# Performance work log

Measured on AMD Instinct MI355X. Metric: run time of the kernel, lower is better.

The kernel has to match this reference:

```python
import jax, jax.numpy as jnp
import numpy as np

N, E, H, L, R, NG = 8192, 131072, 256, 3, 128, 64
NUM_ELEMENTS = 80
CUTOFF = 12.0
INV_SQRT_2 = 1.0 / np.sqrt(2.0)
INV_SQRT_3 = 1.0 / np.sqrt(3.0)
INV_SQRT_H = 1.0 / np.sqrt(H)


def _glorot(key, shape):
    fan_in, fan_out = shape[-2], shape[-1]
    return jax.random.normal(key, shape, jnp.float32) * np.sqrt(2.0 / (fan_in + fan_out))


def setup_inputs():
    key = jax.random.key(0)
    ks = jax.random.split(key, 24)
    pos = jax.random.normal(ks[0], (N, 3), jnp.float32) * 5.0
    z = jax.random.randint(ks[1], (N,), 0, NUM_ELEMENTS)
    src = jax.random.randint(ks[2], (E,), 0, N)
    off = jax.random.randint(ks[3], (E,), 1, N)
    dst = (src + off) % N  # guarantee no self-loops (dist > 0)
    edge_index = jnp.stack([src, dst])
    batch = jnp.sort(jax.random.randint(ks[4], (N,), 0, NG))
    return {
        "pos": pos,
        "atom_emb": jax.random.normal(ks[5], (NUM_ELEMENTS, H), jnp.float32),
        "ln_w": jnp.ones((L, H), jnp.float32),
        "ln_b": jnp.zeros((L, H), jnp.float32),
        "xp_w1": _glorot(ks[6], (L, H, H)),
        "xp_b1": jnp.zeros((L, H), jnp.float32),
        "xp_w2": _glorot(ks[7], (L, H, 3 * H)),
        "xp_b2": jnp.zeros((L, 3 * H), jnp.float32),
        "rbf_w": _glorot(ks[8], (L, R, 3 * H)),
        "rbf_b": jnp.zeros((L, 3 * H), jnp.float32),
        "vec_w": _glorot(ks[9], (L, H, 2 * H)),
        "xv_w1": _glorot(ks[10], (L, 2 * H, H)),
        "xv_b1": jnp.zeros((L, H), jnp.float32),
        "xv_w2": _glorot(ks[11], (L, H, 3 * H)),
        "xv_b2": jnp.zeros((L, 3 * H), jnp.float32),
        "oe_w1": _glorot(ks[12], (H, H // 2)),
        "oe_b1": jnp.zeros((H // 2,), jnp.float32),
        "oe_w2": _glorot(ks[13], (H // 2, 1)),
        "oe_b2": jnp.zeros((1,), jnp.float32),
        "z": z,
        "edge_index": edge_index,
        "batch": batch,
    }


def _gaussian_rbf(dist):
    offset = jnp.linspace(0.0, CUTOFF, R)
    coeff = -0.5 / (offset[1] - offset[0]) ** 2
    return jnp.exp(coeff * (dist[:, None] - offset[None, :]) ** 2)  # [E, R]


def _layernorm(x, w, b):
    mu = x.mean(-1, keepdims=True)
    var = x.var(-1, keepdims=True)
    return (x - mu) / jnp.sqrt(var + 1e-5) * w + b


def reference(pos, atom_emb, ln_w, ln_b, xp_w1, xp_b1, xp_w2, xp_b2,
              rbf_w, rbf_b, vec_w, xv_w1, xv_b1, xv_w2, xv_b2,
              oe_w1, oe_b1, oe_w2, oe_b2, z, edge_index, batch):
    src, dst = edge_index[0], edge_index[1]
    rel = pos[src] - pos[dst]                       # [E, 3]
    dist = jnp.sqrt((rel ** 2).sum(-1))             # [E]
    edge_rbf = _gaussian_rbf(dist)                  # [E, R]
    edge_vector = rel / dist[:, None]               # [E, 3] unit vectors

    x = atom_emb[z]                                 # [N, H]
    vec = jnp.zeros((N, 3, H), x.dtype)

    for l in range(L):
        # ---- PaiNNMessage ----
        xh = _layernorm(x, ln_w[l], ln_b[l])
        xh = jax.nn.silu(xh @ xp_w1[l] + xp_b1[l]) @ xp_w2[l] + xp_b2[l]  # [N, 3H]
        rbfh = edge_rbf @ rbf_w[l] + rbf_b[l]                             # [E, 3H]
        m = xh[src] * rbfh
        mx, xh2, xh3 = jnp.split(m, 3, axis=-1)
        xh2 = xh2 * INV_SQRT_3
        mvec = (vec[src] * xh2[:, None, :] + xh3[:, None, :] * edge_vector[:, :, None]) * INV_SQRT_H
        dx = jax.ops.segment_sum(mx, dst, num_segments=N)
        dvec = jax.ops.segment_sum(mvec, dst, num_segments=N)
        x = (x + dx) * INV_SQRT_2
        vec = vec + dvec

        # ---- PaiNNUpdate ----
        vp = vec @ vec_w[l]                          # [N, 3, 2H]
        vec1, vec2 = jnp.split(vp, 2, axis=-1)
        vec_dot = (vec1 * vec2).sum(axis=1) * INV_SQRT_H           # [N, H]
        vnorm = jnp.sqrt((vec2 ** 2).sum(axis=1) + 1e-8)           # [N, H]
        h = jnp.concatenate([x, vnorm], axis=-1)
        h = jax.nn.silu(h @ xv_w1[l] + xv_b1[l]) @ xv_w2[l] + xv_b2[l]
        xv1, xv2, xv3 = jnp.split(h, 3, axis=-1)
        dx = (xv1 + xv2 * vec_dot) * INV_SQRT_2
        dvec = xv3[:, None, :] * vec1
        x = (x + dx) * INV_SQRT_2
        vec = vec + dvec

    # ---- energy head: per-atom MLP then per-molecule sum ----
    per_atom = jax.nn.silu(x @ oe_w1 + oe_b1) @ oe_w2 + oe_b2      # [N, 1]
    energy = jax.ops.segment_sum(per_atom, batch, num_segments=NG)  # [NG, 1]
    return energy
```

## Files before the change

kernel.cpp:

```cpp
#include <hip/hip_runtime.h>
#include <hip/hip_bf16.h>
#include <math.h>

#define NN 8192
#define EE 131072
#define HH 256
#define LL 3
#define RR 128
#define NGG 64
#define MSG_WAVES 16

typedef __attribute__((ext_vector_type(8))) short bf16x8;
typedef __attribute__((ext_vector_type(4))) float f32x4;
typedef unsigned short u16;

#if defined(__has_builtin)
#if __has_builtin(__builtin_amdgcn_fdot2_f32_bf16)
#define HAVE_FDOT2 1
typedef __attribute__((ext_vector_type(2))) __bf16 bf16x2_t;
union BU { unsigned u; bf16x2_t v; };
#endif
#if __has_builtin(__builtin_amdgcn_global_load_lds)
#define HAVE_GLL 1
#endif
#endif

union U4 { ushort4 v; unsigned short a[4]; };
union U8 { uint4 v; unsigned short a[8]; unsigned w[4]; };

__device__ __forceinline__ float silu(float v) { return v / (1.0f + expf(-v)); }
__device__ __forceinline__ float b2f(unsigned short u) { return __uint_as_float(((unsigned)u) << 16); }
__device__ __forceinline__ unsigned short f2b(float f) {
    unsigned u = __float_as_uint(f);
    u += 0x7fff + ((u >> 16) & 1);
    return (unsigned short)(u >> 16);
}

constexpr float kInvSqrt2 = 0.70710678118654752440f;
constexpr float kInvSqrt3 = 0.57735026918962576451f;
constexpr float kInvSqrtH = 0.0625f;

__global__ void k_zero(float* __restrict__ p, int n4) {
    int i = blockIdx.x * 256 + threadIdx.x;
    if (i < n4) ((float4*)p)[i] = make_float4(0.f, 0.f, 0.f, 0.f);
}

__global__ __launch_bounds__(256) void k_wt_all(
    const float* __restrict__ xp_w1, const float* __restrict__ xp_w2,
    const float* __restrict__ rbf_w, const float* __restrict__ vec_w,
    const float* __restrict__ xv_w1, const float* __restrict__ xv_w2,
    const float* __restrict__ oe_w1,
    u16* __restrict__ xp_w1T, u16* __restrict__ xp_w2T, u16* __restrict__ rbf_wP,
    u16* __restrict__ vec_wT, u16* __restrict__ xv_w1T, u16* __restrict__ xv_w2T,
    u16* __restrict__ oe_w1T) {
    int bid = blockIdx.x;
    const float* src; u16* dst; int K, N, t, pairmode = 0;
    if (bid < 2400) {
        int l = bid / 800, r = bid % 800;
        if (r < 64)       { src = xp_w1 + (size_t)l * 65536;  dst = xp_w1T + (size_t)l * 65536;  K = 256; N = 256; t = r; }
        else if (r < 256) { src = xp_w2 + (size_t)l * 196608; dst = xp_w2T + (size_t)l * 196608; K = 256; N = 768; t = r - 64; }
        else if (r < 352) { src = rbf_w + (size_t)l * 98304;  dst = rbf_wP + (size_t)l * 98304;  K = 128; N = 768; t = r - 256; pairmode = 1; }
        else if (r < 480) { src = vec_w + (size_t)l * 131072; dst = vec_wT + (size_t)l * 131072; K = 256; N = 512; t = r - 352; }
        else if (r < 608) { src = xv_w1 + (size_t)l * 131072; dst = xv_w1T + (size_t)l * 131072; K = 512; N = 256; t = r - 480; }
        else              { src = xv_w2 + (size_t)l * 196608; dst = xv_w2T + (size_t)l * 196608; K = 256; N = 768; t = r - 608; }
    } else {
        src = oe_w1; dst = oe_w1T; K = 256; N = 128; t = bid - 2400;
    }
    int nx = N >> 5;
    int bn = (t % nx) * 32, bk = (t / nx) * 32;
    int tx = threadIdx.x & 31, ty = threadIdx.x >> 5;
    if (pairmode) {
#pragma unroll
        for (int i = 0; i < 32; i += 8) {
            int k = bk + ty + i, n = bn + tx;
            dst[(size_t)(k >> 1) * 1536 + n * 2 + (k & 1)] = f2b(src[(size_t)k * N + n]);
        }
        return;
    }
    __shared__ float tile[32][33];
#pragma unroll
    for (int i = 0; i < 32; i += 8)
        tile[ty + i][tx] = src[(size_t)(bk + ty + i) * N + bn + tx];
    __syncthreads();
#pragma unroll
    for (int i = 0; i < 32; i += 8)
        dst[(size_t)(bn + ty + i) * K + bk + tx] = f2b(tile[tx][ty + i]);
}

__global__ void k_init_ln(const float* __restrict__ emb, const int* __restrict__ z,
                          const float* __restrict__ w, const float* __restrict__ b,
                          float* __restrict__ x, u16* __restrict__ xlnb) {
    int n = blockIdx.x, t = threadIdx.x;
    float v = emb[z[n] * HH + t];
    x[(size_t)n * HH + t] = v;
    float s = v, q = v * v;
#pragma unroll
    for (int m = 32; m >= 1; m >>= 1) {
        s += __shfl_xor(s, m, 64);
        q += __shfl_xor(q, m, 64);
    }
    __shared__ float s_sum[4], s_sq[4];
    int wid = t >> 6;
    if ((t & 63) == 0) { s_sum[wid] = s; s_sq[wid] = q; }
    __syncthreads();
    float S = s_sum[0] + s_sum[1] + s_sum[2] + s_sum[3];
    float Q = s_sq[0] + s_sq[1] + s_sq[2] + s_sq[3];
    float mu = S * (1.0f / HH);
    float var = Q * (1.0f / HH) - mu * mu;
    float rs = rsqrtf(var + 1e-5f);
    xlnb[(size_t)n * HH + t] = f2b((v - mu) * rs * w[t] + b[t]);
}

__global__ void k_geom_hist(const float* __restrict__ pos, const int* __restrict__ ei,
                            float* __restrict__ ev, int* __restrict__ deg) {
    int e = blockIdx.x * 256 + threadIdx.x;
    if (e >= EE) return;
    int s = ei[e], d = ei[EE + e];
    float rx = pos[s * 3 + 0] - pos[d * 3 + 0];
    float ry = pos[s * 3 + 1] - pos[d * 3 + 1];
    float rz = pos[s * 3 + 2] - pos[d * 3 + 2];
    float dist = sqrtf(rx * rx + ry * ry + rz * rz);
    float inv = 1.0f / dist;
    ((float4*)ev)[e] = make_float4(rx * inv, ry * inv, rz * inv, dist);
    atomicAdd(&deg[d], 1);
}

__global__ void k_scan1(const int* __restrict__ deg, int* __restrict__ row_ptr,
                        int* __restrict__ csum) {
    __shared__ int buf[256];
    int t = threadIdx.x, base = blockIdx.x * 256;
    int v = deg[base + t];
    buf[t] = v;
    __syncthreads();
    for (int ofs = 1; ofs < 256; ofs <<= 1) {
        int add = (t >= ofs) ? buf[t - ofs] : 0;
        __syncthreads();
        buf[t] += add;
        __syncthreads();
    }
    row_ptr[base + t] = buf[t] - v;
    if (t == 255) csum[blockIdx.x] = buf[t];
}
__global__ void k_scan2(int* __restrict__ csum) {
    if (threadIdx.x == 0) {
        int acc = 0;
        for (int i = 0; i < 32; ++i) { int v = csum[i]; csum[i] = acc; acc += v; }
        csum[32] = acc;
    }
}
__global__ void k_scan3(const int* __restrict__ csum, int* __restrict__ row_ptr,
                        int* __restrict__ fill) {
    int i = blockIdx.x * 256 + threadIdx.x;
    int v = row_ptr[i] + csum[i >> 8];
    row_ptr[i] = v;
    fill[i] = v;
    if (i == 0) row_ptr[NN] = csum[32];
}

__global__ void k_sort(const int* __restrict__ deg, int* __restrict__ dorder) {
    __shared__ int bins[256];
    __shared__ int base[256];
    int t = threadIdx.x;
    bins[t] = 0;
    __syncthreads();
    for (int d = t; d < NN; d += 256) {
        int b = deg[d]; b = b > 255 ? 255 : b;
        atomicAdd(&bins[b], 1);
    }
    __syncthreads();
    if (t == 0) {
        int acc = 0;
        for (int k = 255; k >= 0; --k) { base[k] = acc; acc += bins[k]; }
    }
    __syncthreads();
    bins[t] = 0;
    __syncthreads();
    for (int d = t; d < NN; d += 256) {
        int b = deg[d]; b = b > 255 ? 255 : b;
        int p = atomicAdd(&bins[b], 1);
        dorder[base[b] + p] = d;
    }
}

__global__ void k_scatter(const int* __restrict__ ei, const float* __restrict__ ev,
                          int* __restrict__ fill, int* __restrict__ srcp,
                          float4* __restrict__ evp, int* __restrict__ kptab,
                          unsigned* __restrict__ gtab) {
    int e = blockIdx.x * 256 + threadIdx.x;
    if (e >= EE) return;
    int d = ei[EE + e];
    int pos = atomicAdd(&fill[d], 1);
    float4 e4 = ((const float4*)ev)[e];
    srcp[pos] = ei[e];
    evp[pos] = e4;
    const float step = 12.0f / 127.0f;
    const float coeff = -0.5f / (step * step);
    float dist = e4.w;
    int k0 = ((int)floorf(dist / step) - 3) & ~1;
    k0 = k0 < 0 ? 0 : (k0 > 120 ? 120 : k0);
    float g[8];
#pragma unroll
    for (int k = 0; k < 8; ++k) {
        float t = dist - (k0 + k) * step;
        g[k] = expf(coeff * t * t);
    }
    kptab[pos] = k0 >> 1;
    unsigned g0 = (unsigned)f2b(g[0]) | ((unsigned)f2b(g[1]) << 16);
    unsigned g1 = (unsigned)f2b(g[2]) | ((unsigned)f2b(g[3]) << 16);
    unsigned g2 = (unsigned)f2b(g[4]) | ((unsigned)f2b(g[5]) << 16);
    unsigned g3 = (unsigned)f2b(g[6]) | ((unsigned)f2b(g[7]) << 16);
    ((uint4*)gtab)[pos] = make_uint4(g0, g1, g2, g3);
}

template <int OUT_BF16, int ACT, int TN>
__global__ __launch_bounds__(256) void k_gemm(
    const u16* __restrict__ A, const u16* __restrict__ BT,
    const float* __restrict__ bias, void* __restrict__ C, int M, int K, int N) {
    __shared__ u16 As[64 * 64];
    __shared__ u16 Bs[TN * 64];
    const int NJ = TN / 32;
    int tid = threadIdx.x;
    int wave = tid >> 6, lane = tid & 63;
    int bm = blockIdx.y * 64, bn = blockIdx.x * TN;
    int wm = (wave & 1) * 32, wn = (wave >> 1) * (TN / 2);
    int lm = lane & 15;
    int kg = lane >> 4;
    f32x4 acc[2][NJ] = {};

    for (int k0 = 0; k0 < K; k0 += 64) {
#pragma unroll
        for (int it = 0; it < 2; ++it) {
            int idx = it * 256 + tid;
            int r = idx >> 3, seg = idx & 7;
#ifdef HAVE_GLL
            __builtin_amdgcn_global_load_lds(
                (const unsigned*)&A[(size_t)(bm + r) * K + k0 + seg * 8],
                (unsigned*)&As[idx * 8], 16, 0, 0);
#else
            *(uint4*)&As[idx * 8] = *(const uint4*)&A[(size_t)(bm + r) * K + k0 + seg * 8];
#endif
        }
#pragma unroll
        for (int it = 0; it < TN / 32; ++it) {
            int idx = it * 256 + tid;
            int r = idx >> 3, seg = idx & 7;
#ifdef HAVE_GLL
            __builtin_amdgcn_global_load_lds(
                (const unsigned*)&BT[(size_t)(bn + r) * K + k0 + seg * 8],
                (unsigned*)&Bs[idx * 8], 16, 0, 0);
#else
            *(uint4*)&Bs[idx * 8] = *(const uint4*)&BT[(size_t)(bn + r) * K + k0 + seg * 8];
#endif
        }
        __syncthreads();
#pragma unroll
        for (int kh = 0; kh < 2; ++kh) {
            bf16x8 af[2], bfr[NJ];
#pragma unroll
            for (int i = 0; i < 2; ++i)
                af[i] = *(const bf16x8*)&As[(wm + i * 16 + lm) * 64 + kh * 32 + kg * 8];
#pragma unroll
            for (int j = 0; j < NJ; ++j)
                bfr[j] = *(const bf16x8*)&Bs[(wn + j * 16 + lm) * 64 + kh * 32 + kg * 8];
#pragma unroll
            for (int i = 0; i < 2; ++i)
#pragma unroll
                for (int j = 0; j < NJ; ++j)
                    acc[i][j] = __builtin_amdgcn_mfma_f32_16x16x32_bf16(af[i], bfr[j], acc[i][j], 0, 0, 0);
        }
        __syncthreads();
    }

#pragma unroll
    for (int j = 0; j < NJ; ++j) {
        int col = bn + wn + j * 16 + lm;
        float bv = bias ? bias[col] : 0.f;
#pragma unroll
        for (int i = 0; i < 2; ++i) {
            int row0 = bm + wm + i * 16 + kg * 4;
#pragma unroll
            for (int r = 0; r < 4; ++r) {
                float v = acc[i][j][r] + bv;
                if (ACT) v = silu(v);
                if (OUT_BF16)
                    ((u16*)C)[(size_t)(row0 + r) * N + col] = f2b(v);
                else
                    ((float*)C)[(size_t)(row0 + r) * N + col] = v;
            }
        }
    }
}

__global__ __launch_bounds__(1024) void k_msg(
    const u16* __restrict__ xhb, const u16* __restrict__ vinb,
    const int* __restrict__ srcp, const float4* __restrict__ evp,
    const int* __restrict__ row_ptr, const int* __restrict__ kptab,
    const unsigned* __restrict__ gtab, const u16* __restrict__ WP ,
    const float* __restrict__ rbias, float* __restrict__ x,
    const float* __restrict__ vin, u16* __restrict__ vecMb,
    const int* __restrict__ dorder) {
    __shared__ u16 Wp[64 * 512];
    int tid = threadIdx.x;
    int wave = tid >> 6, lane = tid & 63;
    int c0 = lane * 4;
    int d = dorder[blockIdx.x * MSG_WAVES + wave];
    int E0 = row_ptr[d], E1 = row_ptr[d + 1];
    float accv[3][4] = {};

#pragma unroll
    for (int p = 0; p < 3; ++p) {
        __syncthreads();
#pragma unroll
        for (int it = 0; it < 4; ++it) {
            int idx = it * 1024 + tid;
            int r = idx >> 6;
            int c8 = (idx & 63) * 8;
            *(uint4*)&Wp[r * 512 + c8] =
                *(const uint4*)&WP[(size_t)r * 1536 + p * 512 + c8];
        }
        __syncthreads();
        float4 bb = ((const float4*)(rbias + p * 256))[lane];
        float bias4[4] = {bb.x, bb.y, bb.z, bb.w};
        float accx[4] = {};

        int kp_n = 0; uint4 gt_n = make_uint4(0, 0, 0, 0);
        U4 X_n; U4 V0_n, V1_n, V2_n; float4 ev_n;
        X_n.v = make_ushort4(0, 0, 0, 0);
        V0_n = X_n; V1_n = X_n; V2_n = X_n;
        ev_n = make_float4(0.f, 0.f, 0.f, 0.f);
        if (E0 < E1) {
            int s0 = srcp[E0];
            kp_n = kptab[E0];
            gt_n = ((const uint4*)gtab)[E0];
            X_n.v = *(const ushort4*)(xhb + (size_t)s0 * 768 + p * 256 + c0);
            if (p == 1) {
                V0_n.v = *(const ushort4*)(vinb + (size_t)s0 * 768 + c0);
                V1_n.v = *(const ushort4*)(vinb + (size_t)s0 * 768 + 256 + c0);
                V2_n.v = *(const ushort4*)(vinb + (size_t)s0 * 768 + 512 + c0);
            }
            if (p == 2) ev_n = evp[E0];
        }
        for (int j = E0; j < E1; ++j) {
            int kp = kp_n;
            uint4 gt = gt_n;
            U4 X = X_n, V0 = V0_n, V1 = V1_n, V2 = V2_n;
            float4 ev4 = ev_n;
            if (j + 1 < E1) {
                int s2 = srcp[j + 1];
                kp_n = kptab[j + 1];
                gt_n = ((const uint4*)gtab)[j + 1];
                X_n.v = *(const ushort4*)(xhb + (size_t)s2 * 768 + p * 256 + c0);
                if (p == 1) {
                    V0_n.v = *(const ushort4*)(vinb + (size_t)s2 * 768 + c0);
                    V1_n.v = *(const ushort4*)(vinb + (size_t)s2 * 768 + 256 + c0);
                    V2_n.v = *(const ushort4*)(vinb + (size_t)s2 * 768 + 512 + c0);
                }
                if (p == 2) ev_n = evp[j + 1];
            }
            unsigned gp0 = gt.x, gp1 = gt.y, gp2 = gt.z, gp3 = gt.w;
            float rr[4] = {bias4[0], bias4[1], bias4[2], bias4[3]};
            {
                U8 w0, w1, w2, w3;
                w0.v = *(const uint4*)&Wp[(kp + 0) * 512 + c0 * 2];
                w1.v = *(const uint4*)&Wp[(kp + 1) * 512 + c0 * 2];
                w2.v = *(const uint4*)&Wp[(kp + 2) * 512 + c0 * 2];
                w3.v = *(const uint4*)&Wp[(kp + 3) * 512 + c0 * 2];
#ifdef HAVE_FDOT2
                BU g0; g0.u = gp0; BU g1; g1.u = gp1;
                BU g2; g2.u = gp2; BU g3; g3.u = gp3;
#pragma unroll
                for (int c = 0; c < 4; ++c) {
                    BU a; a.u = w0.w[c];
                    rr[c] = __builtin_amdgcn_fdot2_f32_bf16(a.v, g0.v, rr[c], false);
                    a.u = w1.w[c];
                    rr[c] = __builtin_amdgcn_fdot2_f32_bf16(a.v, g1.v, rr[c], false);
                    a.u = w2.w[c];
                    rr[c] = __builtin_amdgcn_fdot2_f32_bf16(a.v, g2.v, rr[c], false);
                    a.u = w3.w[c];
                    rr[c] = __builtin_amdgcn_fdot2_f32_bf16(a.v, g3.v, rr[c], false);
                }
#else
                float ge0 = b2f((u16)(gp0 & 0xffff)), go0 = b2f((u16)(gp0 >> 16));
                float ge1 = b2f((u16)(gp1 & 0xffff)), go1 = b2f((u16)(gp1 >> 16));
                float ge2 = b2f((u16)(gp2 & 0xffff)), go2 = b2f((u16)(gp2 >> 16));
                float ge3 = b2f((u16)(gp3 & 0xffff)), go3 = b2f((u16)(gp3 >> 16));
#pragma unroll
                for (int c = 0; c < 4; ++c) {
                    rr[c] += ge0 * b2f(w0.a[2 * c]) + go0 * b2f(w0.a[2 * c + 1]);
                    rr[c] += ge1 * b2f(w1.a[2 * c]) + go1 * b2f(w1.a[2 * c + 1]);
                    rr[c] += ge2 * b2f(w2.a[2 * c]) + go2 * b2f(w2.a[2 * c + 1]);
                    rr[c] += ge3 * b2f(w3.a[2 * c]) + go3 * b2f(w3.a[2 * c + 1]);
                }
#endif
            }
            if (p == 0) {
#pragma unroll
                for (int c = 0; c < 4; ++c) accx[c] += b2f(X.a[c]) * rr[c];
            } else if (p == 1) {
#pragma unroll
                for (int c = 0; c < 4; ++c) {
                    float m1 = b2f(X.a[c]) * rr[c] * kInvSqrt3;
                    accv[0][c] += b2f(V0.a[c]) * m1;
                    accv[1][c] += b2f(V1.a[c]) * m1;
                    accv[2][c] += b2f(V2.a[c]) * m1;
                }
            } else {
#pragma unroll
                for (int c = 0; c < 4; ++c) {
                    float m2 = b2f(X.a[c]) * rr[c];
                    accv[0][c] += m2 * ev4.x;
                    accv[1][c] += m2 * ev4.y;
                    accv[2][c] += m2 * ev4.z;
                }
            }
        }
        if (p == 0) {
            size_t xi = (size_t)d * 256 + c0;
            float4 xv = *(const float4*)&x[xi];
            xv.x = (xv.x + accx[0]) * kInvSqrt2;
            xv.y = (xv.y + accx[1]) * kInvSqrt2;
            xv.z = (xv.z + accx[2]) * kInvSqrt2;
            xv.w = (xv.w + accx[3]) * kInvSqrt2;
            *(float4*)&x[xi] = xv;
        }
    }
#pragma unroll
    for (int k = 0; k < 3; ++k) {
        size_t idx = (size_t)d * 768 + k * 256 + c0;
        float4 vv = *(const float4*)&vin[idx];
        ushort4 u;
        u.x = f2b(vv.x + accv[k][0] * kInvSqrtH);
        u.y = f2b(vv.y + accv[k][1] * kInvSqrtH);
        u.z = f2b(vv.z + accv[k][2] * kInvSqrtH);
        u.w = f2b(vv.w + accv[k][3] * kInvSqrtH);
        *(ushort4*)&vecMb[idx] = u;
    }
}

__global__ void k_vecdot(const u16* __restrict__ vp, const float* __restrict__ x,
                         float* __restrict__ vec_dot, u16* __restrict__ hcat) {
    int idx = blockIdx.x * 256 + threadIdx.x;
    int n = idx >> 5, lg = idx & 31;
    int c0 = lg * 8;
    const u16* p = vp + (size_t)n * 1536;
    float ds[8] = {}, qs[8] = {};
#pragma unroll
    for (int k = 0; k < 3; ++k) {
        uint4 a = *(const uint4*)&p[k * 512 + c0];
        uint4 b = *(const uint4*)&p[k * 512 + 256 + c0];
        const unsigned* aw = (const unsigned*)&a;
        const unsigned* bw = (const unsigned*)&b;
#pragma unroll
        for (int w = 0; w < 4; ++w) {
            float a0 = __uint_as_float(aw[w] << 16);
            float a1 = __uint_as_float(aw[w] & 0xffff0000u);
            float b0 = __uint_as_float(bw[w] << 16);
            float b1 = __uint_as_float(bw[w] & 0xffff0000u);
            ds[2 * w]     += a0 * b0;  qs[2 * w]     += b0 * b0;
            ds[2 * w + 1] += a1 * b1;  qs[2 * w + 1] += b1 * b1;
        }
    }
    size_t vo = (size_t)n * 256 + c0;
    *(float4*)&vec_dot[vo] =
        make_float4(ds[0] * kInvSqrtH, ds[1] * kInvSqrtH, ds[2] * kInvSqrtH, ds[3] * kInvSqrtH);
    *(float4*)&vec_dot[vo + 4] =
        make_float4(ds[4] * kInvSqrtH, ds[5] * kInvSqrtH, ds[6] * kInvSqrtH, ds[7] * kInvSqrtH);
    float4 x0 = *(const float4*)&x[vo];
    float4 x1 = *(const float4*)&x[vo + 4];
    *(ushort4*)&hcat[(size_t)n * 512 + c0] =
        make_ushort4(f2b(x0.x), f2b(x0.y), f2b(x0.z), f2b(x0.w));
    *(ushort4*)&hcat[(size_t)n * 512 + c0 + 4] =
        make_ushort4(f2b(x1.x), f2b(x1.y), f2b(x1.z), f2b(x1.w));
    *(ushort4*)&hcat[(size_t)n * 512 + 256 + c0] =
        make_ushort4(f2b(sqrtf(qs[0] + 1e-8f)), f2b(sqrtf(qs[1] + 1e-8f)),
                     f2b(sqrtf(qs[2] + 1e-8f)), f2b(sqrtf(qs[3] + 1e-8f)));
    *(ushort4*)&hcat[(size_t)n * 512 + 256 + c0 + 4] =
        make_ushort4(f2b(sqrtf(qs[4] + 1e-8f)), f2b(sqrtf(qs[5] + 1e-8f)),
                     f2b(sqrtf(qs[6] + 1e-8f)), f2b(sqrtf(qs[7] + 1e-8f)));
}

__global__ void k_update_out(const u16* __restrict__ hout, const float* __restrict__ vec_dot,
                             const u16* __restrict__ vp, float* __restrict__ x,
                             const u16* __restrict__ vecMb, float* __restrict__ vfin,
                             u16* __restrict__ vb,
                             const float* __restrict__ lnw, const float* __restrict__ lnb,
                             u16* __restrict__ xout) {
    int idx = blockIdx.x * 256 + threadIdx.x;
    int n = idx >> 5, lg = idx & 31;
    int c0 = lg * 8;
    size_t hb = (size_t)n * 768;
    uint4 H1 = *(const uint4*)&hout[hb + c0];
    uint4 H2 = *(const uint4*)&hout[hb + 256 + c0];
    uint4 H3 = *(const uint4*)&hout[hb + 512 + c0];
    const unsigned* h1w = (const unsigned*)&H1;
    const unsigned* h2w = (const unsigned*)&H2;
    const unsigned* h3w = (const unsigned*)&H3;
    size_t xo = (size_t)n * 256 + c0;
    float4 vd0 = *(const float4*)&vec_dot[xo];
    float4 vd1 = *(const float4*)&vec_dot[xo + 4];
    float vd[8] = {vd0.x, vd0.y, vd0.z, vd0.w, vd1.x, vd1.y, vd1.z, vd1.w};
    float4 x0 = *(const float4*)&x[xo];
    float4 x1 = *(const float4*)&x[xo + 4];
    float xv[8] = {x0.x, x0.y, x0.z, x0.w, x1.x, x1.y, x1.z, x1.w};
    float nx[8], xv3[8];
#pragma unroll
    for (int w = 0; w < 4; ++w) {
        float a1 = __uint_as_float(h1w[w] << 16), b1 = __uint_as_float(h1w[w] & 0xffff0000u);
        float a2 = __uint_as_float(h2w[w] << 16), b2v = __uint_as_float(h2w[w] & 0xffff0000u);
        nx[2 * w]     = (xv[2 * w]     + (a1 + a2  * vd[2 * w])     * kInvSqrt2) * kInvSqrt2;
        nx[2 * w + 1] = (xv[2 * w + 1] + (b1 + b2v * vd[2 * w + 1]) * kInvSqrt2) * kInvSqrt2;
        xv3[2 * w]     = __uint_as_float(h3w[w] << 16);
        xv3[2 * w + 1] = __uint_as_float(h3w[w] & 0xffff0000u);
    }
    *(float4*)&x[xo]     = make_float4(nx[0], nx[1], nx[2], nx[3]);
    *(float4*)&x[xo + 4] = make_float4(nx[4], nx[5], nx[6], nx[7]);
#pragma unroll
    for (int k = 0; k < 3; ++k) {
        size_t vo = hb + k * 256 + c0;
        uint4 VM = *(const uint4*)&vecMb[vo];
        uint4 VP = *(const uint4*)&vp[(size_t)n * 1536 + k * 512 + c0];
        const unsigned* vmw = (const unsigned*)&VM;
        const unsigned* vpw = (const unsigned*)&VP;
        float nv[8];
#pragma unroll
        for (int w = 0; w < 4; ++w) {
            nv[2 * w]     = __uint_as_float(vmw[w] << 16)
                          + xv3[2 * w]     * __uint_as_float(vpw[w] << 16);
            nv[2 * w + 1] = __uint_as_float(vmw[w] & 0xffff0000u)
                          + xv3[2 * w + 1] * __uint_as_float(vpw[w] & 0xffff0000u);
        }
        *(float4*)&vfin[vo]     = make_float4(nv[0], nv[1], nv[2], nv[3]);
        *(float4*)&vfin[vo + 4] = make_float4(nv[4], nv[5], nv[6], nv[7]);
        *(ushort4*)&vb[vo]     = make_ushort4(f2b(nv[0]), f2b(nv[1]), f2b(nv[2]), f2b(nv[3]));
        *(ushort4*)&vb[vo + 4] = make_ushort4(f2b(nv[4]), f2b(nv[5]), f2b(nv[6]), f2b(nv[7]));
    }
    if (lnw) {
        float s = 0.f, q = 0.f;
#pragma unroll
        for (int c = 0; c < 8; ++c) { s += nx[c]; q += nx[c] * nx[c]; }
#pragma unroll
        for (int m = 16; m >= 1; m >>= 1) {
            s += __shfl_xor(s, m, 64);
            q += __shfl_xor(q, m, 64);
        }
        float mu = s * (1.0f / HH);
        float var = q * (1.0f / HH) - mu * mu;
        float rs = rsqrtf(var + 1e-5f);
        float4 w0 = *(const float4*)&lnw[c0], w1 = *(const float4*)&lnw[c0 + 4];
        float4 bb0 = *(const float4*)&lnb[c0], bb1 = *(const float4*)&lnb[c0 + 4];
        float lw[8] = {w0.x, w0.y, w0.z, w0.w, w1.x, w1.y, w1.z, w1.w};
        float lb[8] = {bb0.x, bb0.y, bb0.z, bb0.w, bb1.x, bb1.y, bb1.z, bb1.w};
        u16 o[8];
#pragma unroll
        for (int c = 0; c < 8; ++c) o[c] = f2b((nx[c] - mu) * rs * lw[c] + lb[c]);
        *(ushort4*)&xout[xo]     = make_ushort4(o[0], o[1], o[2], o[3]);
        *(ushort4*)&xout[xo + 4] = make_ushort4(o[4], o[5], o[6], o[7]);
    } else {
        *(ushort4*)&xout[xo]     = make_ushort4(f2b(nx[0]), f2b(nx[1]), f2b(nx[2]), f2b(nx[3]));
        *(ushort4*)&xout[xo + 4] = make_ushort4(f2b(nx[4]), f2b(nx[5]), f2b(nx[6]), f2b(nx[7]));
    }
}

__global__ void k_energy2(const float* __restrict__ h, const float* __restrict__ w2,
                          const float* __restrict__ b2, const int* __restrict__ batch,
                          float* __restrict__ out) {
    __shared__ float g[NGG];
    int t = threadIdx.x;
    if (t < NGG) g[t] = 0.f;
    __syncthreads();
    int a = blockIdx.x * 256 + t;
    const float4* hr = (const float4*)(h + (size_t)a * 128);
    const float4* w4 = (const float4*)w2;
    float acc = 0.f;
#pragma unroll 8
    for (int i = 0; i < 32; ++i) {
        float4 hv = hr[i], wv = w4[i];
        acc += hv.x * wv.x + hv.y * wv.y + hv.z * wv.z + hv.w * wv.w;
    }
    acc += b2[0];
    atomicAdd(&g[batch[a]], acc);
    __syncthreads();
    if (t < NGG && g[t] != 0.f) atomicAdd(&out[t], g[t]);
}

extern "C" void kernel_launch(void* const* d_in, const int* in_sizes, int n_in,
                              void* d_out, int out_size, void* d_ws, size_t ws_size,
                              hipStream_t stream) {
    const float* pos      = (const float*)d_in[0];
    const float* atom_emb = (const float*)d_in[1];
    const float* ln_w     = (const float*)d_in[2];
    const float* ln_b     = (const float*)d_in[3];
    const float* xp_w1    = (const float*)d_in[4];
    const float* xp_b1    = (const float*)d_in[5];
    const float* xp_w2    = (const float*)d_in[6];
    const float* xp_b2    = (const float*)d_in[7];
    const float* rbf_w    = (const float*)d_in[8];
    const float* rbf_b    = (const float*)d_in[9];
    const float* vec_w    = (const float*)d_in[10];
    const float* xv_w1    = (const float*)d_in[11];
    const float* xv_b1    = (const float*)d_in[12];
    const float* xv_w2    = (const float*)d_in[13];
    const float* xv_b2    = (const float*)d_in[14];
    const float* oe_w1    = (const float*)d_in[15];
    const float* oe_b1    = (const float*)d_in[16];
    const float* oe_w2    = (const float*)d_in[17];
    const float* oe_b2    = (const float*)d_in[18];
    const int*   z        = (const int*)d_in[19];
    const int*   ei       = (const int*)d_in[20];
    const int*   batch    = (const int*)d_in[21];
    float* out = (float*)d_out;

    char* ws = (char*)d_ws;
    size_t off = 0;
    auto alloc = [&](size_t b) {
        void* p = ws + off;
        off = (off + b + 255) & ~(size_t)255;
        return p;
    };
    float*    x      = (float*)alloc((size_t)NN * HH * 4);
    float*    vecA   = (float*)alloc((size_t)NN * 768 * 4);
    u16*      vb     = (u16*)alloc((size_t)NN * 768 * 2);
    u16*      vecMb  = (u16*)alloc((size_t)NN * 768 * 2);
    u16*      xlnb   = (u16*)alloc((size_t)NN * HH * 2);
    u16*      t1b    = (u16*)alloc((size_t)NN * HH * 2);
    u16*      xhb    = (u16*)alloc((size_t)NN * 768 * 2);
    float*    vdot   = (float*)alloc((size_t)NN * HH * 4);
    u16*      vpb    = (u16*)alloc((size_t)NN * 1536 * 2);
    u16*      houtb  = (u16*)alloc((size_t)NN * 768 * 2);
    float*    ev     = (float*)alloc((size_t)EE * 4 * 4);
    int*      deg    = (int*)alloc((size_t)NN * 4);
    int*      row_ptr= (int*)alloc((size_t)(NN + 1) * 4);
    int*      fill   = (int*)alloc((size_t)NN * 4);
    int*      dorder = (int*)alloc((size_t)NN * 4);
    int*      csum   = (int*)alloc((size_t)33 * 4);
    int*      srcp   = (int*)alloc((size_t)EE * 4);
    float4*   evp    = (float4*)alloc((size_t)EE * 16);
    int*      kptab  = (int*)alloc((size_t)EE * 4);
    unsigned* gtab   = (unsigned*)alloc((size_t)EE * 16);
    u16* xp_w1T   = (u16*)alloc((size_t)3 * 256 * 256 * 2);
    u16* xp_w2T   = (u16*)alloc((size_t)3 * 768 * 256 * 2);
    u16* rbf_wP   = (u16*)alloc((size_t)3 * 128 * 768 * 2);
    u16* vec_wT   = (u16*)alloc((size_t)3 * 512 * 256 * 2);
    u16* xv_w1T   = (u16*)alloc((size_t)3 * 256 * 512 * 2);
    u16* xv_w2T   = (u16*)alloc((size_t)3 * 768 * 256 * 2);
    u16* oe_w1T   = (u16*)alloc((size_t)128 * 256 * 2);
    (void)ws_size;

    u16*   h1b   = t1b;
    u16*   hcatb = xhb;
    float* heng  = vdot;
    u16*   xb    = xlnb;

    k_wt_all<<<2432, 256, 0, stream>>>(xp_w1, xp_w2, rbf_w, vec_w, xv_w1, xv_w2, oe_w1,
                                       xp_w1T, xp_w2T, rbf_wP, vec_wT, xv_w1T, xv_w2T, oe_w1T);
    k_zero<<<(36 * 1024 * 1024 / 16 + 255) / 256, 256, 0, stream>>>(vecA, 36 * 1024 * 1024 / 16);
    k_zero<<<8, 256, 0, stream>>>((float*)deg, NN / 4);
    k_init_ln<<<NN, 256, 0, stream>>>(atom_emb, z, ln_w, ln_b, x, xlnb);
    k_geom_hist<<<EE / 256, 256, 0, stream>>>(pos, ei, ev, deg);
    k_scan1<<<32, 256, 0, stream>>>(deg, row_ptr, csum);
    k_scan2<<<1, 64, 0, stream>>>(csum);
    k_scan3<<<32, 256, 0, stream>>>(csum, row_ptr, fill);
    k_sort<<<1, 256, 0, stream>>>(deg, dorder);
    k_scatter<<<EE / 256, 256, 0, stream>>>(ei, ev, fill, srcp, evp, kptab, gtab);

    for (int l = 0; l < LL; ++l) {
        k_gemm<1, 1, 64><<<dim3(4, NN / 64), 256, 0, stream>>>(
            xlnb, xp_w1T + (size_t)l * 256 * 256, xp_b1 + l * HH, t1b, NN, 256, 256);
        k_gemm<1, 0, 128><<<dim3(6, NN / 64), 256, 0, stream>>>(
            t1b, xp_w2T + (size_t)l * 768 * 256, xp_b2 + l * 768, xhb, NN, 256, 768);
        k_msg<<<NN / MSG_WAVES, 1024, 0, stream>>>(
            xhb, vb, srcp, evp, row_ptr, kptab, gtab,
            rbf_wP + (size_t)l * 128 * 768, rbf_b + l * 768, x, vecA, vecMb, dorder);

        k_gemm<1, 0, 128><<<dim3(4, 3 * NN / 64), 256, 0, stream>>>(
            vecMb, vec_wT + (size_t)l * 512 * 256, nullptr, vpb, 3 * NN, 256, 512);
        k_vecdot<<<NN / 8, 256, 0, stream>>>(vpb, x, vdot, hcatb);
        k_gemm<1, 1, 64><<<dim3(4, NN / 64), 256, 0, stream>>>(
            hcatb, xv_w1T + (size_t)l * 256 * 512, xv_b1 + l * HH, h1b, NN, 512, 256);
        k_gemm<1, 0, 128><<<dim3(6, NN / 64), 256, 0, stream>>>(
            h1b, xv_w2T + (size_t)l * 768 * 256, xv_b2 + l * 768, houtb, NN, 256, 768);
        bool last = (l == LL - 1);
        k_update_out<<<NN / 8, 256, 0, stream>>>(
            houtb, vdot, vpb, x, vecMb, vecA, vb,
            last ? nullptr : ln_w + (l + 1) * HH,
            last ? nullptr : ln_b + (l + 1) * HH, xlnb);
    }

    k_gemm<0, 1, 64><<<dim3(2, NN / 64), 256, 0, stream>>>(
        xb, oe_w1T, oe_b1, heng, NN, 256, 128);
    k_zero<<<1, 256, 0, stream>>>(out, NGG / 4);
    k_energy2<<<32, 256, 0, stream>>>(heng, oe_w2, oe_b2, batch, out);
}
```

Baseline: 711.7 us.

## Use 64x64 GEMM tiles with K=256 swizzled LDS staging; halve message block size

The GEMM kernel now uses a fixed 64x64 output tile and stages a full 256-wide K slice of A and B in LDS, with an XOR swizzle on 16-byte segments to avoid bank conflicts. This cuts the number of barriers and K-loop iterations, and it launches more blocks for the wide GEMMs. The message-passing kernel switches from 16 to 8 waves per block (512 threads), so each block processes fewer destination nodes. In exchange, the GEMM uses 64 KB of LDS per block, which may lower occupancy, and each smaller message block reloads the rbf weight slice into LDS, amortizing that load over fewer nodes.

Result: slower. 727.5 us (+2.2%).

```diff
diff --git a/kernel.cpp b/kernel.cpp
--- a/kernel.cpp
+++ b/kernel.cpp
@@ -8,7 +8,7 @@
 #define LL 3
 #define RR 128
 #define NGG 64
-#define MSG_WAVES 16
+#define MSG_WAVES 8
 
 typedef __attribute__((ext_vector_type(8))) short bf16x8;
 typedef __attribute__((ext_vector_type(4))) float f32x4;
@@ -212,67 +212,74 @@
     ((uint4*)gtab)[pos] = make_uint4(g0, g1, g2, g3);
 }
 
-template <int OUT_BF16, int ACT, int TN>
+template <int OUT_BF16, int ACT>
 __global__ __launch_bounds__(256) void k_gemm(
     const u16* __restrict__ A, const u16* __restrict__ BT,
     const float* __restrict__ bias, void* __restrict__ C, int M, int K, int N) {
-    __shared__ u16 As[64 * 64];
-    __shared__ u16 Bs[TN * 64];
-    const int NJ = TN / 32;
+    __shared__ u16 As[64 * 256];
+    __shared__ u16 Bs[64 * 256];
     int tid = threadIdx.x;
     int wave = tid >> 6, lane = tid & 63;
-    int bm = blockIdx.y * 64, bn = blockIdx.x * TN;
-    int wm = (wave & 1) * 32, wn = (wave >> 1) * (TN / 2);
+    int bm = blockIdx.y * 64, bn = blockIdx.x * 64;
+    int wm = (wave & 1) * 32, wn = (wave >> 1) * 32;
     int lm = lane & 15;
     int kg = lane >> 4;
-    f32x4 acc[2][NJ] = {};
-
-    for (int k0 = 0; k0 < K; k0 += 64) {
-#pragma unroll
-        for (int it = 0; it < 2; ++it) {
+    f32x4 acc[2][2] = {};
+
+    for (int k0 = 0; k0 < K; k0 += 256) {
+#pragma unroll
+        for (int it = 0; it < 8; ++it) {
             int idx = it * 256 + tid;
-            int r = idx >> 3, seg = idx & 7;
+            int r = idx >> 5;
+            int lseg = (idx & 31) ^ (r & 7);
 #ifdef HAVE_GLL
             __builtin_amdgcn_global_load_lds(
-                (const unsigned*)&A[(size_t)(bm + r) * K + k0 + seg * 8],
+                (const unsigned*)&A[(size_t)(bm + r) * K + k0 + lseg * 8],
                 (unsigned*)&As[idx * 8], 16, 0, 0);
 #else
-            *(uint4*)&As[idx * 8] = *(const uint4*)&A[(size_t)(bm + r) * K + k0 + seg * 8];
+            *(uint4*)&As[idx * 8] = *(const uint4*)&A[(size_t)(bm + r) * K + k0 + lseg * 8];
 #endif
         }
 #pragma unroll
-        for (int it = 0; it < TN / 32; ++it) {
+        for (int it = 0; it < 8; ++it) {
             int idx = it * 256 + tid;
-            int r = idx >> 3, seg = idx & 7;
+            int r = idx >> 5;
+            int lseg = (idx & 31) ^ (r & 7);
 #ifdef HAVE_GLL
             __builtin_amdgcn_global_load_lds(
-                (const unsigned*)&BT[(size_t)(bn + r) * K + k0 + seg * 8],
+                (const unsigned*)&BT[(size_t)(bn + r) * K + k0 + lseg * 8],
                 (unsigned*)&Bs[idx * 8], 16, 0, 0);
 #else
-            *(uint4*)&Bs[idx * 8] = *(const uint4*)&BT[(size_t)(bn + r) * K + k0 + seg * 8];
+            *(uint4*)&Bs[idx * 8] = *(const uint4*)&BT[(size_t)(bn + r) * K + k0 + lseg * 8];
 #endif
         }
         __syncthreads();
 #pragma unroll
-        for (int kh = 0; kh < 2; ++kh) {
-            bf16x8 af[2], bfr[NJ];
+        for (int ks = 0; ks < 8; ++ks) {
+            bf16x8 af[2], bfr[2];
+#pragma unroll
+            for (int i = 0; i < 2; ++i) {
+                int row = wm + i * 16 + lm;
+                int pseg = (ks * 4 + kg) ^ (row & 7);
+                af[i] = *(const bf16x8*)&As[row * 256 + pseg * 8];
+            }
+#pragma unroll
+            for (int j = 0; j < 2; ++j) {
+                int row = wn + j * 16 + lm;
+                int pseg = (ks * 4 + kg) ^ (row & 7);
+                bfr[j] = *(const bf16x8*)&Bs[row * 256 + pseg * 8];
+            }
 #pragma unroll
             for (int i = 0; i < 2; ++i)
-                af[i] = *(const bf16x8*)&As[(wm + i * 16 + lm) * 64 + kh * 32 + kg * 8];
-#pragma unroll
-            for (int j = 0; j < NJ; ++j)
-                bfr[j] = *(const bf16x8*)&Bs[(wn + j * 16 + lm) * 64 + kh * 32 + kg * 8];
-#pragma unroll
-            for (int i = 0; i < 2; ++i)
-#pragma unroll
-                for (int j = 0; j < NJ; ++j)
+#pragma unroll
+                for (int j = 0; j < 2; ++j)
                     acc[i][j] = __builtin_amdgcn_mfma_f32_16x16x32_bf16(af[i], bfr[j], acc[i][j], 0, 0, 0);
         }
-        __syncthreads();
-    }
-
-#pragma unroll
-    for (int j = 0; j < NJ; ++j) {
+        if (k0 + 256 < K) __syncthreads();
+    }
+
+#pragma unroll
+    for (int j = 0; j < 2; ++j) {
         int col = bn + wn + j * 16 + lm;
         float bv = bias ? bias[col] : 0.f;
 #pragma unroll
@@ -291,7 +298,7 @@
     }
 }
 
-__global__ __launch_bounds__(1024) void k_msg(
+__global__ __launch_bounds__(512) void k_msg(
     const u16* __restrict__ xhb, const u16* __restrict__ vinb,
     const int* __restrict__ srcp, const float4* __restrict__ evp,
     const int* __restrict__ row_ptr, const int* __restrict__ kptab,
@@ -311,8 +318,8 @@
     for (int p = 0; p < 3; ++p) {
         __syncthreads();
 #pragma unroll
-        for (int it = 0; it < 4; ++it) {
-            int idx = it * 1024 + tid;
+        for (int it = 0; it < 8; ++it) {
+            int idx = it * 512 + tid;
             int r = idx >> 6;
             int c8 = (idx & 63) * 8;
             *(uint4*)&Wp[r * 512 + c8] =
@@ -664,20 +671,20 @@
     k_scatter<<<EE / 256, 256, 0, stream>>>(ei, ev, fill, srcp, evp, kptab, gtab);
 
     for (int l = 0; l < LL; ++l) {
-        k_gemm<1, 1, 64><<<dim3(4, NN / 64), 256, 0, stream>>>(
+        k_gemm<1, 1><<<dim3(4, NN / 64), 256, 0, stream>>>(
             xlnb, xp_w1T + (size_t)l * 256 * 256, xp_b1 + l * HH, t1b, NN, 256, 256);
-        k_gemm<1, 0, 128><<<dim3(6, NN / 64), 256, 0, stream>>>(
+        k_gemm<1, 0><<<dim3(12, NN / 64), 256, 0, stream>>>(
             t1b, xp_w2T + (size_t)l * 768 * 256, xp_b2 + l * 768, xhb, NN, 256, 768);
-        k_msg<<<NN / MSG_WAVES, 1024, 0, stream>>>(
+        k_msg<<<NN / MSG_WAVES, 64 * MSG_WAVES, 0, stream>>>(
             xhb, vb, srcp, evp, row_ptr, kptab, gtab,
             rbf_wP + (size_t)l * 128 * 768, rbf_b + l * 768, x, vecA, vecMb, dorder);
 
-        k_gemm<1, 0, 128><<<dim3(4, 3 * NN / 64), 256, 0, stream>>>(
+        k_gemm<1, 0><<<dim3(8, 3 * NN / 64), 256, 0, stream>>>(
             vecMb, vec_wT + (size_t)l * 512 * 256, nullptr, vpb, 3 * NN, 256, 512);
         k_vecdot<<<NN / 8, 256, 0, stream>>>(vpb, x, vdot, hcatb);
-        k_gemm<1, 1, 64><<<dim3(4, NN / 64), 256, 0, stream>>>(
+        k_gemm<1, 1><<<dim3(4, NN / 64), 256, 0, stream>>>(
             hcatb, xv_w1T + (size_t)l * 256 * 512, xv_b1 + l * HH, h1b, NN, 512, 256);
-        k_gemm<1, 0, 128><<<dim3(6, NN / 64), 256, 0, stream>>>(
+        k_gemm<1, 0><<<dim3(12, NN / 64), 256, 0, stream>>>(
             h1b, xv_w2T + (size_t)l * 768 * 256, xv_b2 + l * 768, houtb, NN, 256, 768);
         bool last = (l == LL - 1);
         k_update_out<<<NN / 8, 256, 0, stream>>>(
@@ -686,7 +693,7 @@
             last ? nullptr : ln_b + (l + 1) * HH, xlnb);
     }
 
-    k_gemm<0, 1, 64><<<dim3(2, NN / 64), 256, 0, stream>>>(
+    k_gemm<0, 1><<<dim3(2, NN / 64), 256, 0, stream>>>(
         xb, oe_w1T, oe_b1, heng, NN, 256, 128);
     k_zero<<<1, 256, 0, stream>>>(out, NGG / 4);
     k_energy2<<<32, 256, 0, stream>>>(heng, oe_w2, oe_b2, batch, out);
```
